# Kernel tuning notes

Measured on AMD Instinct MI355X. Metric: run time of the kernel, lower is better.

## Reference

```python
import jax, jax.numpy as jnp
import numpy as np

VOCAB, EMBED, HIDDEN = 32000, 256, 64
B, T = 4096, 64


def setup_inputs() -> dict:
    key = jax.random.key(0)
    ks = jax.random.split(key, 6)
    s = 1.0 / float(np.sqrt(HIDDEN))  # PyTorch LSTM init scale
    x = jax.random.randint(ks[0], (B, T), 0, VOCAB)
    embed_table = jax.random.normal(ks[1], (VOCAB, EMBED), jnp.float32)
    W_ih = jax.random.uniform(ks[2], (4 * HIDDEN, EMBED), jnp.float32, -s, s)
    W_hh = jax.random.uniform(ks[3], (4 * HIDDEN, HIDDEN), jnp.float32, -s, s)
    b_ih = jax.random.uniform(ks[4], (4 * HIDDEN,), jnp.float32, -s, s)
    b_hh = jax.random.uniform(ks[5], (4 * HIDDEN,), jnp.float32, -s, s)
    return {"x": x, "embed_table": embed_table, "W_ih": W_ih, "W_hh": W_hh, "b_ih": b_ih, "b_hh": b_hh}


def reference(x, embed_table, W_ih, W_hh, b_ih, b_hh):
    # Embedding lookup: [B,T,E]
    emb = embed_table[x]
    # Precompute input projection for all timesteps (PyTorch gate order i,f,g,o)
    xg = jnp.einsum('bte,ge->btg', emb, W_ih) + (b_ih + b_hh)  # [B,T,4H]
    xg = jnp.swapaxes(xg, 0, 1)  # [T,B,4H]
    h0 = jnp.zeros((x.shape[0], HIDDEN), xg.dtype)
    c0 = jnp.zeros((x.shape[0], HIDDEN), xg.dtype)

    def step(carry, xt):
        h, c = carry
        g = xt + h @ W_hh.T  # [B,4H]
        i, f, gg, o = jnp.split(g, 4, axis=-1)
        c = jax.nn.sigmoid(f) * c + jax.nn.sigmoid(i) * jnp.tanh(gg)
        h = jax.nn.sigmoid(o) * jnp.tanh(c)
        return (h, c), None

    (h, _), _ = jax.lax.scan(step, (h0, c0), xg)
    return h  # [B, HIDDEN] == hidden.squeeze(0)
```

## Files before the change

kernel.cpp:

```cpp
#include <hip/hip_runtime.h>
#include <math.h>

#define B_ 4096
#define T_ 64
#define E_ 256
#define H_ 64
#define THREADS 768

typedef __attribute__((ext_vector_type(8))) short bf16x8;
typedef __attribute__((ext_vector_type(4))) float f32x4;
typedef __attribute__((ext_vector_type(4))) unsigned int u32x4;

__device__ __forceinline__ unsigned cvt_pk_bf16(float lo, float hi) {
    unsigned r;
    asm("v_cvt_pk_bf16_f32 %0, %1, %2" : "=v"(r) : "v"(lo), "v"(hi));
    return r;
}
__device__ __forceinline__ float exp2_raw(float x) {
    float r; asm("v_exp_f32 %0, %1" : "=v"(r) : "v"(x)); return r;
}
__device__ __forceinline__ float rcp_raw(float x) {
    float r; asm("v_rcp_f32 %0, %1" : "=v"(r) : "v"(x)); return r;
}
#define LOG2E 1.442695041f

template <int CTRL>
__device__ __forceinline__ float dpp_f(float x) {
    return __int_as_float(
        __builtin_amdgcn_mov_dpp(__float_as_int(x), CTRL, 0xF, 0xF, true));
}

__device__ __forceinline__ bf16x8 pack8(const float* q) {
    float4 f0 = *(const float4*)q;
    float4 f1 = *(const float4*)(q + 4);
    u32x4 w;
    w[0] = cvt_pk_bf16(f0.x, f0.y);
    w[1] = cvt_pk_bf16(f0.z, f0.w);
    w[2] = cvt_pk_bf16(f1.x, f1.y);
    w[3] = cvt_pk_bf16(f1.z, f1.w);
    union { u32x4 u; bf16x8 s; } cvt;
    cvt.u = w;
    return cvt.s;
}

__global__ __attribute__((amdgpu_flat_work_group_size(THREADS, THREADS),
                          amdgpu_waves_per_eu(3, 3)))
void lstm_k(const int* __restrict__ x,
            const float* __restrict__ emb,
            const float* __restrict__ W_ih,
            const float* __restrict__ W_hh,
            const float* __restrict__ b_ih,
            const float* __restrict__ b_hh,
            float* __restrict__ out) {
    __shared__ __align__(16) short s_ef[4][4096];
    __shared__ __align__(16) short s_hf[2][1024];
    __shared__ int s_idx[1024];

    const int tid  = threadIdx.x;
    const int lane = tid & 63;
    const int wave = tid >> 6;
    const int r0   = blockIdx.x * 16;

    for (int i = tid; i < 1024; i += THREADS)
        s_idx[(i & 63) * 16 + (i >> 6)] = x[(r0 + (i >> 6)) * T_ + (i & 63)];
    for (int i = tid; i < 1024; i += THREADS)
        ((int*)s_hf)[i] = 0;

    const int p  = lane & 1;
    const int c4 = lane >> 4;
    const int u  = (lane & 15) >> 1;
    const float scl2 = p ? 1.0f : 2.0f;
    const float offB = p ? 0.0f : -1.0f;
    const float enB  = -LOG2E * scl2;
    const int m0 = c4 * 4 + p * 2;

    bf16x8 wA[8], wB[8], qA0, qA1, qB0, qB1;
    float bA = 0.f, bB = 0.f;
    int hw_s = 0;
    if (wave < 8) {
        const int gA = p * 64 + wave * 8 + u;
        const float* wi0 = W_ih + (size_t)gA * E_;
        const float* wi1 = W_ih + (size_t)(128 + gA) * E_;
        #pragma unroll
        for (int kc = 0; kc < 8; ++kc) {
            wA[kc] = pack8(wi0 + kc * 32 + c4 * 8);
            wB[kc] = pack8(wi1 + kc * 32 + c4 * 8);
        }
        const float* qh0 = W_hh + (size_t)gA * H_ + c4 * 8;
        const float* qh1 = W_hh + (size_t)(128 + gA) * H_ + c4 * 8;
        qA0 = pack8(qh0);
        qA1 = pack8(qh0 + 32);
        qB0 = pack8(qh1);
        qB1 = pack8(qh1 + 32);
        bA = b_ih[gA] + b_hh[gA];
        bB = b_ih[gA + 128] + b_hh[gA + 128];
        hw_s = (wave >> 2) * 512 + (wave & 3) * 128
             + ((u & 1) ? (m0 + 1) * 8 + (u - 1) : m0 * 8 + u);
    }

    const int m16    = lane & 15;
    const int kc0    = (wave - 8) * 2;
    const int sbase0 = kc0 * 512 + lane * 8;
    const int skoff0 = kc0 * 32 + (lane >> 4) * 8;

    __syncthreads();

    if (wave >= 8) {
        #pragma unroll
        for (int tt = 0; tt < 3; ++tt) {
            int tok = s_idx[tt * 16 + m16];
            const float* pr = emb + (size_t)tok * E_;
            #pragma unroll
            for (int kk = 0; kk < 2; ++kk) {
                const float* q = pr + skoff0 + kk * 32;
                float4 f0 = *(const float4*)q;
                float4 f1 = *(const float4*)(q + 4);
                u32x4 w;
                w[0] = cvt_pk_bf16(f0.x, f0.y);
                w[1] = cvt_pk_bf16(f0.z, f0.w);
                w[2] = cvt_pk_bf16(f1.x, f1.y);
                w[3] = cvt_pk_bf16(f1.z, f1.w);
                *(u32x4*)(&s_ef[tt][0] + sbase0 + kk * 512) = w;
            }
        }
    }
    __syncthreads();

    float c0 = 0.f, c1 = 0.f, h0v = 0.f, h1v = 0.f;
    f32x4 a0, a1, b0, b1;

    if (wave < 8) {
        a0 = (f32x4){bA, bA, bA, bA};
        b0 = (f32x4){bB, bB, bB, bB};
        a1 = (f32x4){0.f, 0.f, 0.f, 0.f};
        b1 = (f32x4){0.f, 0.f, 0.f, 0.f};
        const short* eb = &s_ef[0][0] + lane * 8;
        #pragma unroll
        for (int kc = 0; kc < 4; ++kc) {
            bf16x8 av = *(const bf16x8*)(eb + kc * 512);
            bf16x8 aw = *(const bf16x8*)(eb + (kc + 4) * 512);
            a0 = __builtin_amdgcn_mfma_f32_16x16x32_bf16(av, wA[kc], a0, 0, 0, 0);
            b0 = __builtin_amdgcn_mfma_f32_16x16x32_bf16(av, wB[kc], b0, 0, 0, 0);
            a1 = __builtin_amdgcn_mfma_f32_16x16x32_bf16(aw, wA[kc + 4], a1, 0, 0, 0);
            b1 = __builtin_amdgcn_mfma_f32_16x16x32_bf16(aw, wB[kc + 4], b1, 0, 0, 0);
        }
    }

    auto gates_phase = [&](const float* ga, const float* gb, int t) {
        float sA[4], Bv[4];
        #pragma unroll
        for (int q = 0; q < 4; ++q) {
            sA[q] = rcp_raw(1.0f + exp2_raw(-LOG2E * ga[q]));
            Bv[q] = rcp_raw(1.0f + exp2_raw(enB * gb[q])) * scl2 + offB;
        }
        float s1 = p ? sA[0] : sA[2] * Bv[2];
        float r1 = dpp_f<0xB1>(s1);
        float s2 = p ? sA[1] : sA[3] * Bv[3];
        float r2 = dpp_f<0xB1>(s2);
        float r3 = dpp_f<0xB1>(Bv[0]);
        float r4 = dpp_f<0xB1>(Bv[1]);
        float fc0 = p ? sA[2] : r1;
        float ic0 = p ? r1 : sA[0] * Bv[0];
        float oc0 = p ? Bv[2] : r3;
        float fc1 = p ? sA[3] : r2;
        float ic1 = p ? r2 : sA[1] * Bv[1];
        float oc1 = p ? Bv[3] : r4;
        c0 = fc0 * c0 + ic0;
        c1 = fc1 * c1 + ic1;
        h0v = oc0 * (1.0f - 2.0f * rcp_raw(1.0f + exp2_raw(2.0f * LOG2E * c0)));
        h1v = oc1 * (1.0f - 2.0f * rcp_raw(1.0f + exp2_raw(2.0f * LOG2E * c1)));
        float snd = (u & 1) ? h0v : h1v;
        float rcv = dpp_f<0x4E>(snd);
        unsigned hw = (u & 1) ? cvt_pk_bf16(rcv, h1v) : cvt_pk_bf16(h0v, rcv);
        *(unsigned*)(&s_hf[(t + 1) & 1][0] + hw_s) = hw;
    };

    auto p_phase = [&](int t) {
        a0 = (f32x4){bA, bA, bA, bA};
        b0 = (f32x4){bB, bB, bB, bB};
        a1 = (f32x4){0.f, 0.f, 0.f, 0.f};
        b1 = (f32x4){0.f, 0.f, 0.f, 0.f};
        const short* eb = &s_ef[(t + 1) & 3][0] + lane * 8;
        __builtin_amdgcn_s_setprio(1);
        #pragma unroll
        for (int kc = 0; kc < 4; ++kc) {
            bf16x8 av = *(const bf16x8*)(eb + kc * 512);
            bf16x8 aw = *(const bf16x8*)(eb + (kc + 4) * 512);
            a0 = __builtin_amdgcn_mfma_f32_16x16x32_bf16(av, wA[kc], a0, 0, 0, 0);
            b0 = __builtin_amdgcn_mfma_f32_16x16x32_bf16(av, wB[kc], b0, 0, 0, 0);
            a1 = __builtin_amdgcn_mfma_f32_16x16x32_bf16(aw, wA[kc + 4], a1, 0, 0, 0);
            b1 = __builtin_amdgcn_mfma_f32_16x16x32_bf16(aw, wB[kc + 4], b1, 0, 0, 0);
        }
        __builtin_amdgcn_s_setprio(0);
    };

    #pragma unroll 4
    for (int t = 0; t < T_; ++t) {
        if (wave < 8) {
            const short* hb = &s_hf[t & 1][0] + lane * 8;
            bf16x8 hv0 = *(const bf16x8*)(hb);
            bf16x8 hv1 = *(const bf16x8*)(hb + 512);
            __builtin_amdgcn_s_setprio(1);
            a0 = __builtin_amdgcn_mfma_f32_16x16x32_bf16(hv0, qA0, a0, 0, 0, 0);
            a1 = __builtin_amdgcn_mfma_f32_16x16x32_bf16(hv1, qA1, a1, 0, 0, 0);
            b0 = __builtin_amdgcn_mfma_f32_16x16x32_bf16(hv0, qB0, b0, 0, 0, 0);
            b1 = __builtin_amdgcn_mfma_f32_16x16x32_bf16(hv1, qB1, b1, 0, 0, 0);
            __builtin_amdgcn_s_setprio(0);

            float ga[4], gb[4];
            #pragma unroll
            for (int q = 0; q < 4; ++q) {
                ga[q] = a0[q] + a1[q];
                gb[q] = b0[q] + b1[q];
            }

            if (wave < 4) {
                gates_phase(ga, gb, t);
                if (t < T_ - 1) p_phase(t);
            } else {
                __builtin_amdgcn_sched_barrier(0);
                if (t < T_ - 1) p_phase(t);
                __builtin_amdgcn_sched_barrier(0);
                gates_phase(ga, gb, t);
            }
        } else {
            if (t + 3 < T_) {
                int tok = s_idx[(t + 3) * 16 + m16];
                const float* pr = emb + (size_t)tok * E_;
                #pragma unroll
                for (int kk = 0; kk < 2; ++kk) {
                    const float* q = pr + skoff0 + kk * 32;
                    float4 f0 = *(const float4*)q;
                    float4 f1 = *(const float4*)(q + 4);
                    u32x4 w;
                    w[0] = cvt_pk_bf16(f0.x, f0.y);
                    w[1] = cvt_pk_bf16(f0.z, f0.w);
                    w[2] = cvt_pk_bf16(f1.x, f1.y);
                    w[3] = cvt_pk_bf16(f1.z, f1.w);
                    *(u32x4*)(&s_ef[(t + 3) & 3][0] + sbase0 + kk * 512) = w;
                }
            }
        }
        __syncthreads();
    }

    if (wave < 8) {
        const int j = wave * 8 + u;
        out[(r0 + m0) * H_ + j]     = h0v;
        out[(r0 + m0 + 1) * H_ + j] = h1v;
    }
}

extern "C" void kernel_launch(void* const* d_in, const int* in_sizes, int n_in,
                              void* d_out, int out_size, void* d_ws, size_t ws_size,
                              hipStream_t stream) {
    const int*   x         = (const int*)d_in[0];
    const float* emb_table = (const float*)d_in[1];
    const float* W_ih      = (const float*)d_in[2];
    const float* W_hh      = (const float*)d_in[3];
    const float* b_ih      = (const float*)d_in[4];
    const float* b_hh      = (const float*)d_in[5];
    float*       out       = (float*)d_out;

    lstm_k<<<B_ / 16, THREADS, 0, stream>>>(x, emb_table, W_ih, W_hh,
                                            b_ih, b_hh, out);
}
```

Measured before the change: 75.21 us.

## Pre-convert embedding table to bf16 and gather rows directly into LDS

Adds a prep kernel that converts the whole fp32 embedding table to bf16 in the workspace on every call. The LSTM kernel then gathers embedding rows with global_load_lds straight into shared memory, skipping the register round-trip and per-element conversion. It also replaces the full syncthreads with a partial vmcnt wait, so the newest prefetch stays in flight across the barrier. This halves the bytes moved by the gather, at the cost of a full-table read and write pass over the table before the main kernel runs.

```diff
diff --git a/kernel.cpp b/kernel.cpp
--- a/kernel.cpp
+++ b/kernel.cpp
@@ -5,6 +5,7 @@
 #define T_ 64
 #define E_ 256
 #define H_ 64
+#define V_ 32000
 #define THREADS 768
 
 typedef __attribute__((ext_vector_type(8))) short bf16x8;
@@ -43,10 +44,34 @@
     return cvt.s;
 }
 
+__device__ __forceinline__ void gld16(const void* g, void* l) {
+    __builtin_amdgcn_global_load_lds(
+        (const __attribute__((address_space(1))) void*)g,
+        (__attribute__((address_space(3))) void*)l, 16, 0, 0);
+}
+
+__global__ void prep_tab(const float* __restrict__ emb_table,
+                         short* __restrict__ emb_bf, int tabN) {
+    int tid = blockIdx.x * blockDim.x + threadIdx.x;
+    int stride = gridDim.x * blockDim.x;
+    for (int i = tid; i < (tabN >> 3); i += stride) {
+        float4 v0 = ((const float4*)emb_table)[i * 2];
+        float4 v1 = ((const float4*)emb_table)[i * 2 + 1];
+        u32x4 w;
+        w[0] = cvt_pk_bf16(v0.x, v0.y);
+        w[1] = cvt_pk_bf16(v0.z, v0.w);
+        w[2] = cvt_pk_bf16(v1.x, v1.y);
+        w[3] = cvt_pk_bf16(v1.z, v1.w);
+        ((u32x4*)emb_bf)[i] = w;
+    }
+}
+
+template <int TAB>
 __global__ __attribute__((amdgpu_flat_work_group_size(THREADS, THREADS),
                           amdgpu_waves_per_eu(3, 3)))
-void lstm_k(const int* __restrict__ x,
-            const float* __restrict__ emb,
+void lstm_f(const int* __restrict__ x,
+            const float* __restrict__ embf,
+            const short* __restrict__ embb,
             const float* __restrict__ W_ih,
             const float* __restrict__ W_hh,
             const float* __restrict__ b_ih,
@@ -102,6 +127,7 @@
     const int kc0    = (wave - 8) * 2;
     const int sbase0 = kc0 * 512 + lane * 8;
     const int skoff0 = kc0 * 32 + (lane >> 4) * 8;
+    const int skoff1 = skoff0 + 32;
 
     __syncthreads();
 
@@ -109,22 +135,33 @@
         #pragma unroll
         for (int tt = 0; tt < 3; ++tt) {
             int tok = s_idx[tt * 16 + m16];
-            const float* pr = emb + (size_t)tok * E_;
-            #pragma unroll
-            for (int kk = 0; kk < 2; ++kk) {
-                const float* q = pr + skoff0 + kk * 32;
-                float4 f0 = *(const float4*)q;
-                float4 f1 = *(const float4*)(q + 4);
-                u32x4 w;
-                w[0] = cvt_pk_bf16(f0.x, f0.y);
-                w[1] = cvt_pk_bf16(f0.z, f0.w);
-                w[2] = cvt_pk_bf16(f1.x, f1.y);
-                w[3] = cvt_pk_bf16(f1.z, f1.w);
-                *(u32x4*)(&s_ef[tt][0] + sbase0 + kk * 512) = w;
+            if (TAB) {
+                gld16(embb + (size_t)tok * E_ + skoff0, &s_ef[tt][kc0 * 512]);
+                gld16(embb + (size_t)tok * E_ + skoff1, &s_ef[tt][kc0 * 512 + 512]);
+            } else {
+                const float* pr = embf + (size_t)tok * E_;
+                #pragma unroll
+                for (int kk = 0; kk < 2; ++kk) {
+                    const float* q = pr + skoff0 + kk * 32;
+                    float4 f0 = *(const float4*)q;
+                    float4 f1 = *(const float4*)(q + 4);
+                    u32x4 w;
+                    w[0] = cvt_pk_bf16(f0.x, f0.y);
+                    w[1] = cvt_pk_bf16(f0.z, f0.w);
+                    w[2] = cvt_pk_bf16(f1.x, f1.y);
+                    w[3] = cvt_pk_bf16(f1.z, f1.w);
+                    *(u32x4*)(&s_ef[tt][0] + sbase0 + kk * 512) = w;
+                }
             }
         }
     }
-    __syncthreads();
+    if (TAB) {
+        asm volatile("s_waitcnt vmcnt(2) lgkmcnt(0)" ::: "memory");
+        __builtin_amdgcn_s_barrier();
+        __builtin_amdgcn_sched_barrier(0);
+    } else {
+        __syncthreads();
+    }
 
     float c0 = 0.f, c1 = 0.f, h0v = 0.f, h1v = 0.f;
     f32x4 a0, a1, b0, b1;
@@ -226,22 +263,35 @@
         } else {
             if (t + 3 < T_) {
                 int tok = s_idx[(t + 3) * 16 + m16];
-                const float* pr = emb + (size_t)tok * E_;
-                #pragma unroll
-                for (int kk = 0; kk < 2; ++kk) {
-                    const float* q = pr + skoff0 + kk * 32;
-                    float4 f0 = *(const float4*)q;
-                    float4 f1 = *(const float4*)(q + 4);
-                    u32x4 w;
-                    w[0] = cvt_pk_bf16(f0.x, f0.y);
-                    w[1] = cvt_pk_bf16(f0.z, f0.w);
-                    w[2] = cvt_pk_bf16(f1.x, f1.y);
-                    w[3] = cvt_pk_bf16(f1.z, f1.w);
-                    *(u32x4*)(&s_ef[(t + 3) & 3][0] + sbase0 + kk * 512) = w;
+                if (TAB) {
+                    gld16(embb + (size_t)tok * E_ + skoff0,
+                          &s_ef[(t + 3) & 3][kc0 * 512]);
+                    gld16(embb + (size_t)tok * E_ + skoff1,
+                          &s_ef[(t + 3) & 3][kc0 * 512 + 512]);
+                } else {
+                    const float* pr = embf + (size_t)tok * E_;
+                    #pragma unroll
+                    for (int kk = 0; kk < 2; ++kk) {
+                        const float* q = pr + skoff0 + kk * 32;
+                        float4 f0 = *(const float4*)q;
+                        float4 f1 = *(const float4*)(q + 4);
+                        u32x4 w;
+                        w[0] = cvt_pk_bf16(f0.x, f0.y);
+                        w[1] = cvt_pk_bf16(f0.z, f0.w);
+                        w[2] = cvt_pk_bf16(f1.x, f1.y);
+                        w[3] = cvt_pk_bf16(f1.z, f1.w);
+                        *(u32x4*)(&s_ef[(t + 3) & 3][0] + sbase0 + kk * 512) = w;
+                    }
                 }
             }
         }
-        __syncthreads();
+        if (TAB) {
+            asm volatile("s_waitcnt vmcnt(2) lgkmcnt(0)" ::: "memory");
+            __builtin_amdgcn_s_barrier();
+            __builtin_amdgcn_sched_barrier(0);
+        } else {
+            __syncthreads();
+        }
     }
 
     if (wave < 8) {
@@ -262,6 +312,16 @@
     const float* b_hh      = (const float*)d_in[5];
     float*       out       = (float*)d_out;
 
-    lstm_k<<<B_ / 16, THREADS, 0, stream>>>(x, emb_table, W_ih, W_hh,
-                                            b_ih, b_hh, out);
-}
+    short* emb_bf = (short*)d_ws;
+    const size_t need = (size_t)V_ * E_ * 2;
+    const int tab = (ws_size >= need) ? 1 : 0;
+
+    if (tab) {
+        prep_tab<<<2048, 256, 0, stream>>>(emb_table, emb_bf, V_ * E_);
+        lstm_f<1><<<B_ / 16, THREADS, 0, stream>>>(
+            x, emb_table, emb_bf, W_ih, W_hh, b_ih, b_hh, out);
+    } else {
+        lstm_f<0><<<B_ / 16, THREADS, 0, stream>>>(
+            x, emb_table, (const short*)d_ws, W_ih, W_hh, b_ih, b_hh, out);
+    }
+}
```

Result: faster. 69.94 us (-7.0%).
